# Kernel tuning notes

Hardware: AMD Instinct MI355X
Metric: run time of the kernel (lower is better)

## Reference

```python
import jax, jax.numpy as jnp
import numpy as np

EMBED_DIM = 1024
N_HEADS = 16
HEAD_DIM = EMBED_DIM // N_HEADS
B, S = 2, 2048


def setup_inputs() -> dict:
    key = jax.random.key(0)
    ks = jax.random.split(key, 8)
    scale = 1.0 / np.sqrt(EMBED_DIM)
    return {
        "key": jax.random.normal(ks[0], (B, S, EMBED_DIM), jnp.float32),
        "query": jax.random.normal(ks[1], (B, S, EMBED_DIM), jnp.float32),
        "value": jax.random.normal(ks[2], (B, S, EMBED_DIM), jnp.float32),
        # nn.Linear weights stored [out_features, in_features], applied as x @ W.T
        "Wq": jax.random.normal(ks[3], (EMBED_DIM, EMBED_DIM), jnp.float32) * scale,
        "Wk": jax.random.normal(ks[4], (EMBED_DIM, EMBED_DIM), jnp.float32) * scale,
        "Wv": jax.random.normal(ks[5], (EMBED_DIM, EMBED_DIM), jnp.float32) * scale,
        "Wo": jax.random.normal(ks[6], (EMBED_DIM, EMBED_DIM), jnp.float32) * scale,
        "bo": jax.random.normal(ks[7], (EMBED_DIM,), jnp.float32) * scale,
    }


def reference(key, query, value, Wq, Wk, Wv, Wo, bo) -> jnp.ndarray:
    b = key.shape[0]
    # project and split heads: [B, S, E] -> [B, H, S, D]
    def split_heads(x):
        return x.reshape(b, -1, N_HEADS, HEAD_DIM).transpose(0, 2, 1, 3)
    q = split_heads(query @ Wq.T)
    k = split_heads(key @ Wk.T)
    v = split_heads(value @ Wv.T)
    scores = jnp.einsum("bhqd,bhkd->bhqk", q, k) / np.sqrt(HEAD_DIM)
    attn = jax.nn.softmax(scores, axis=-1)
    ctx = jnp.einsum("bhqk,bhkd->bhqd", attn, v)  # [B, H, S, D]
    ctx = ctx.transpose(0, 2, 1, 3).reshape(b, -1, EMBED_DIM)
    return ctx @ Wo.T + bo
```

## Files before the change

### kernel.cpp

```cpp
#include <hip/hip_runtime.h>

typedef unsigned short u16;
typedef __bf16 bf8 __attribute__((ext_vector_type(8)));
typedef __bf16 bf2 __attribute__((ext_vector_type(2)));
typedef float f4 __attribute__((ext_vector_type(4)));

typedef __attribute__((address_space(1))) const unsigned int gas_u32;
typedef __attribute__((address_space(3))) unsigned int las_u32;
#define ASYNC16(g, l) __builtin_amdgcn_global_load_lds((gas_u32*)(g), (las_u32*)(l), 16, 0, 0)

__device__ __forceinline__ unsigned pkbf(float lo, float hi) {
    union { bf2 v; unsigned u; } t;
    t.v[0] = (__bf16)lo;
    t.v[1] = (__bf16)hi;
    return t.u;
}

__device__ __forceinline__ u16 bf1(float f) {
    union { __bf16 v; u16 u; } t;
    t.v = (__bf16)f;
    return t.u;
}

__device__ __forceinline__ float fexp2(float x) {
#if __has_builtin(__builtin_amdgcn_exp2f)
  return __builtin_amdgcn_exp2f(x);
#else
  return __expf(x * 0.69314718056f);
#endif
}

__global__ __launch_bounds__(256) void cvt_all(
    const float* __restrict__ k_, const float* __restrict__ q_, const float* __restrict__ v_,
    const float* __restrict__ wq, const float* __restrict__ wk, const float* __restrict__ wv,
    const float* __restrict__ wo, u16* __restrict__ ws) {
  size_t e = ((size_t)blockIdx.x * 256 + threadIdx.x) * 8;
  const float* src;
  if      (e <  4194304) src = k_ + e;
  else if (e <  8388608) src = q_ + (e - 4194304);
  else if (e < 12582912) src = v_ + (e - 8388608);
  else if (e < 13631488) src = wq + (e - 12582912);
  else if (e < 14680064) src = wk + (e - 13631488);
  else if (e < 15728640) src = wv + (e - 14680064);
  else                   src = wo + (e - 15728640);
  float4 f0 = ((const float4*)src)[0];
  float4 f1 = ((const float4*)src)[1];
  uint4 o;
  o.x = pkbf(f0.x, f0.y);
  o.y = pkbf(f0.z, f0.w);
  o.z = pkbf(f1.x, f1.y);
  o.w = pkbf(f1.z, f1.w);
  *(uint4*)(ws + e) = o;
}

template<int BM, bool FINAL>
__device__ __forceinline__ void gemm_tile(const u16* __restrict__ A, const u16* __restrict__ Bm,
                                          u16* __restrict__ Cb, float* __restrict__ Cf,
                                          const float* __restrict__ bias, float scale,
                                          int bm, int bn, int ldc) {
  __shared__ u16 As[BM*64];
  __shared__ u16 Bs[128*64];
  const int tid = threadIdx.x;
  const int wave = tid >> 6, lane = tid & 63;
  const int wm = wave >> 1, wn = wave & 1;
  const int quad = lane >> 4, l16 = lane & 15;
  const int MI = BM / 32;

  f4 acc[MI][4];
  const f4 zz = {0.f, 0.f, 0.f, 0.f};
  #pragma unroll
  for (int i = 0; i < MI; i++)
    #pragma unroll
    for (int j = 0; j < 4; j++) acc[i][j] = zz;

  const int kr = tid >> 3;
  const int cs = (tid & 7) ^ (kr & 7);
  const u16* ga = A  + (size_t)(bm*BM  + kr)*1024 + cs*8;
  const u16* gb = Bm + (size_t)(bn*128 + kr)*1024 + cs*8;
  u16* la = As + tid*8;
  u16* lb = Bs + tid*8;

  for (int kt = 0; kt < 1024; kt += 64) {
    #pragma unroll
    for (int p = 0; p < BM/32; p++) ASYNC16(ga + (size_t)(p*32)*1024 + kt, la + p*2048);
    #pragma unroll
    for (int p = 0; p < 4; p++)     ASYNC16(gb + (size_t)(p*32)*1024 + kt, lb + p*2048);
    __syncthreads();
    #pragma unroll
    for (int kk = 0; kk < 2; kk++) {
      bf8 af[MI];
      #pragma unroll
      for (int mi = 0; mi < MI; mi++)
        af[mi] = *(const bf8*)(As + (wm*(BM/2) + mi*16 + l16)*64 + (((kk*4 + quad) ^ (l16 & 7))*8));
      #pragma unroll
      for (int ni = 0; ni < 4; ni++) {
        bf8 bfr = *(const bf8*)(Bs + (wn*64 + ni*16 + l16)*64 + (((kk*4 + quad) ^ (l16 & 7))*8));
        #pragma unroll
        for (int mi = 0; mi < MI; mi++)
          acc[mi][ni] = __builtin_amdgcn_mfma_f32_16x16x32_bf16(af[mi], bfr, acc[mi][ni], 0, 0, 0);
      }
    }
    __syncthreads();
  }

  #pragma unroll
  for (int mi = 0; mi < MI; mi++)
    #pragma unroll
    for (int ni = 0; ni < 4; ni++) {
      const int col = bn*128 + wn*64 + ni*16 + l16;
      #pragma unroll
      for (int r = 0; r < 4; r++) {
        const int row = bm*BM + wm*(BM/2) + mi*16 + quad*4 + r;
        if (FINAL) Cf[(size_t)row*ldc + col] = acc[mi][ni][r] + bias[col];
        else       Cb[(size_t)row*ldc + col] = bf1(acc[mi][ni][r] * scale);
      }
    }
}

#define QSCALE 0.180336880f

__global__ __launch_bounds__(256, 3) void gemm_qkv(
    const u16* __restrict__ xq, const u16* __restrict__ xk, const u16* __restrict__ xv,
    const u16* __restrict__ wq, const u16* __restrict__ wk, const u16* __restrict__ wv,
    u16* __restrict__ Qo, u16* __restrict__ Ko, u16* __restrict__ Vto) {
  if (blockIdx.z == 0)
    gemm_tile<128,false>(xq, wq, Qo, nullptr, nullptr, QSCALE, blockIdx.x, blockIdx.y, 1024);
  else if (blockIdx.z == 1)
    gemm_tile<128,false>(xk, wk, Ko, nullptr, nullptr, 1.0f, blockIdx.x, blockIdx.y, 1024);
  else
    gemm_tile<128,false>(wv, xv, Vto, nullptr, nullptr, 1.0f, blockIdx.y, blockIdx.x, 4096);
}

__global__ __launch_bounds__(256, 2) void gemm_out(
    const u16* __restrict__ ctx, const u16* __restrict__ wo,
    const float* __restrict__ bias, float* __restrict__ out) {
  gemm_tile<64,true>(ctx, wo, nullptr, out, bias, 1.0f, blockIdx.x, blockIdx.y, 1024);
}

__global__ __launch_bounds__(256, 4) void flash_attn(
    const u16* __restrict__ Qg, const u16* __restrict__ Kg,
    const u16* __restrict__ Vtg, u16* __restrict__ ctx) {
  __shared__ uint4 smem4[2208];
  u16* Ks = (u16*)smem4;
  u16* Vt = (u16*)smem4 + 8192;
  float* Of = (float*)smem4;
  float* Lf = (float*)smem4 + 2*64*68;

  const int tid = threadIdx.x;
  const int wave = tid >> 6, lane = tid & 63;
  const int quad = lane >> 4, l16 = lane & 15;
  const int wq = wave >> 1, wk = wave & 1;
  const int h = blockIdx.x, qt = blockIdx.y, b = blockIdx.z;

  bf8 qf[2][2];
  {
    const u16* qp = Qg + (size_t)(b*2048 + qt*64 + wq*32)*1024 + h*64;
    #pragma unroll
    for (int qs = 0; qs < 2; qs++)
      #pragma unroll
      for (int kc = 0; kc < 2; kc++)
        qf[qs][kc] = *(const bf8*)(qp + (size_t)(qs*16 + l16)*1024 + kc*32 + quad*8);
  }

  const f4 zz = {0.f, 0.f, 0.f, 0.f};
  f4 ot[4][2];
  float lrow[2] = {0.f, 0.f};
  #pragma unroll
  for (int ds = 0; ds < 4; ds++)
    #pragma unroll
    for (int qs = 0; qs < 2; qs++) ot[ds][qs] = zz;

  const int kr = tid >> 3;
  const u16* kga = Kg + (size_t)(b*2048 + kr)*1024 + h*64 + ((tid & 7) ^ (kr & 7))*8;
  const int vd = tid >> 4;
  const u16* vga = Vtg + (size_t)(h*64 + vd)*4096 + b*2048 + (((tid & 15) ^ vd))*8;
  u16* kld = Ks + tid*8;
  u16* vld = Vt + tid*8;

  const int prow0 = ((l16 >> 2) << 3) + (l16 & 3);
  const int prow1 = prow0 + 4;

  for (int kv0 = 0; kv0 < 2048; kv0 += 128) {
    __syncthreads();
    #pragma unroll
    for (int p = 0; p < 4; p++) ASYNC16(kga + (size_t)(kv0 + p*32)*1024, kld + p*2048);
    #pragma unroll
    for (int p = 0; p < 4; p++) ASYNC16(vga + (size_t)(p*16)*4096 + kv0, vld + p*2048);
    __syncthreads();

    #pragma unroll
    for (int kb = 0; kb < 2; kb++) {
      f4 st[2][2];
      #pragma unroll
      for (int f = 0; f < 2; f++)
        #pragma unroll
        for (int qs = 0; qs < 2; qs++) st[f][qs] = zz;
      __builtin_amdgcn_s_setprio(1);
      #pragma unroll
      for (int f = 0; f < 2; f++) {
        const int row = wk*64 + kb*32 + (f ? prow1 : prow0);
        #pragma unroll
        for (int kc = 0; kc < 2; kc++) {
          bf8 kf = *(const bf8*)(Ks + row*64 + (((kc*4 + quad) ^ (row & 7))*8));
          #pragma unroll
          for (int qs = 0; qs < 2; qs++)
            st[f][qs] = __builtin_amdgcn_mfma_f32_16x16x32_bf16(kf, qf[qs][kc], st[f][qs], 0, 0, 0);
        }
      }
      __builtin_amdgcn_s_setprio(0);
      bf8 pf[2];
      #pragma unroll
      for (int qs = 0; qs < 2; qs++) {
        float p0 = fexp2(st[0][qs][0]), p1 = fexp2(st[0][qs][1]);
        float p2 = fexp2(st[0][qs][2]), p3 = fexp2(st[0][qs][3]);
        float p4 = fexp2(st[1][qs][0]), p5 = fexp2(st[1][qs][1]);
        float p6 = fexp2(st[1][qs][2]), p7 = fexp2(st[1][qs][3]);
        lrow[qs] += ((p0 + p1) + (p2 + p3)) + ((p4 + p5) + (p6 + p7));
        union { uint4 u; bf8 v; } pu;
        pu.u.x = pkbf(p0, p1);
        pu.u.y = pkbf(p2, p3);
        pu.u.z = pkbf(p4, p5);
        pu.u.w = pkbf(p6, p7);
        pf[qs] = pu.v;
      }
      __builtin_amdgcn_s_setprio(1);
      #pragma unroll
      for (int ds = 0; ds < 4; ds++) {
        const int d = ds*16 + l16;
        bf8 vf = *(const bf8*)(Vt + d*128 + (((wk*8 + kb*4 + quad) ^ l16)*8));
        #pragma unroll
        for (int qs = 0; qs < 2; qs++)
          ot[ds][qs] = __builtin_amdgcn_mfma_f32_16x16x32_bf16(vf, pf[qs], ot[ds][qs], 0, 0, 0);
      }
      __builtin_amdgcn_s_setprio(0);
    }
  }

  __syncthreads();
  #pragma unroll
  for (int qs = 0; qs < 2; qs++) {
    lrow[qs] += __shfl_xor(lrow[qs], 16);
    lrow[qs] += __shfl_xor(lrow[qs], 32);
  }
  float* Ofw = Of + wk*(64*68);
  #pragma unroll
  for (int ds = 0; ds < 4; ds++)
    #pragma unroll
    for (int qs = 0; qs < 2; qs++)
      #pragma unroll
      for (int r = 0; r < 4; r++)
        Ofw[(wq*32 + qs*16 + l16)*68 + ds*16 + quad*4 + r] = ot[ds][qs][r];
  if (quad == 0) {
    Lf[wk*64 + wq*32 + l16]      = lrow[0];
    Lf[wk*64 + wq*32 + 16 + l16] = lrow[1];
  }
  __syncthreads();
  {
    const int qr = tid >> 2, dp = (tid & 3)*16;
    const float inv = 1.f / (Lf[qr] + Lf[64 + qr]);
    const float* o0 = Of + qr*68 + dp;
    const float* o1 = o0 + 64*68;
    unsigned ow[8];
    #pragma unroll
    for (int i = 0; i < 8; i++)
      ow[i] = pkbf((o0[2*i] + o1[2*i]) * inv, (o0[2*i+1] + o1[2*i+1]) * inv);
    u16* cp = ctx + (size_t)(b*2048 + qt*64 + qr)*1024 + h*64 + dp;
    *(uint4*)cp       = *(uint4*)&ow[0];
    *(uint4*)(cp + 8) = *(uint4*)&ow[4];
  }
}

extern "C" void kernel_launch(void* const* d_in, const int* in_sizes, int n_in,
                              void* d_out, int out_size, void* d_ws, size_t ws_size,
                              hipStream_t stream) {
  const float* key_  = (const float*)d_in[0];
  const float* query = (const float*)d_in[1];
  const float* value = (const float*)d_in[2];
  const float* Wq = (const float*)d_in[3];
  const float* Wk = (const float*)d_in[4];
  const float* Wv = (const float*)d_in[5];
  const float* Wo = (const float*)d_in[6];
  const float* bo = (const float*)d_in[7];
  float* out = (float*)d_out;

  u16* ws  = (u16*)d_ws;
  u16* xkb = ws;
  u16* xqb = ws + 4194304;
  u16* xvb = ws + 8388608;
  u16* Wqb = ws + 12582912;
  u16* Wkb = ws + 13631488;
  u16* Wvb = ws + 14680064;
  u16* Wob = ws + 15728640;
  u16* Qb  = ws + 16777216;
  u16* Kb  = ws + 20971520;
  u16* Vtb = ws + 25165824;
  u16* Cb  = ws + 29360128;

  cvt_all<<<8192, 256, 0, stream>>>(key_, query, value, Wq, Wk, Wv, Wo, ws);
  gemm_qkv<<<dim3(32, 8, 3), 256, 0, stream>>>(xqb, xkb, xvb, Wqb, Wkb, Wvb, Qb, Kb, Vtb);
  flash_attn<<<dim3(16, 32, 2), 256, 0, stream>>>(Qb, Kb, Vtb, Cb);
  gemm_out<<<dim3(64, 8), 256, 0, stream>>>(Cb, Wob, bo, out);
}
```

Measured before the change: 203.1 us.

## Load K and V fragments directly from global memory into registers in flash attention

Removes the LDS staging of K and V tiles, along with the block-wide barriers around each tile load. Each wave now reads its own K and V MFMA fragments straight from global memory into registers, in a loop unrolled by two to overlap loads with compute. The aim is to cut LDS traffic and synchronisation. In exchange, the four waves of a block no longer share K/V tiles, so global and L2 reads rise and latency hiding now depends on the compiler's scheduling.

```diff
diff --git a/kernel.cpp b/kernel.cpp
--- a/kernel.cpp
+++ b/kernel.cpp
@@ -140,11 +140,9 @@
 __global__ __launch_bounds__(256, 4) void flash_attn(
     const u16* __restrict__ Qg, const u16* __restrict__ Kg,
     const u16* __restrict__ Vtg, u16* __restrict__ ctx) {
-  __shared__ uint4 smem4[2208];
-  u16* Ks = (u16*)smem4;
-  u16* Vt = (u16*)smem4 + 8192;
-  float* Of = (float*)smem4;
-  float* Lf = (float*)smem4 + 2*64*68;
+  __shared__ float Os[2*64*68 + 128];
+  float* Of = Os;
+  float* Lf = Os + 2*64*68;
 
   const int tid = threadIdx.x;
   const int wave = tid >> 6, lane = tid & 63;
@@ -170,73 +168,63 @@
     #pragma unroll
     for (int qs = 0; qs < 2; qs++) ot[ds][qs] = zz;
 
-  const int kr = tid >> 3;
-  const u16* kga = Kg + (size_t)(b*2048 + kr)*1024 + h*64 + ((tid & 7) ^ (kr & 7))*8;
-  const int vd = tid >> 4;
-  const u16* vga = Vtg + (size_t)(h*64 + vd)*4096 + b*2048 + (((tid & 15) ^ vd))*8;
-  u16* kld = Ks + tid*8;
-  u16* vld = Vt + tid*8;
-
   const int prow0 = ((l16 >> 2) << 3) + (l16 & 3);
-  const int prow1 = prow0 + 4;
-
-  for (int kv0 = 0; kv0 < 2048; kv0 += 128) {
-    __syncthreads();
-    #pragma unroll
-    for (int p = 0; p < 4; p++) ASYNC16(kga + (size_t)(kv0 + p*32)*1024, kld + p*2048);
-    #pragma unroll
-    for (int p = 0; p < 4; p++) ASYNC16(vga + (size_t)(p*16)*4096 + kv0, vld + p*2048);
-    __syncthreads();
-
-    #pragma unroll
-    for (int kb = 0; kb < 2; kb++) {
-      f4 st[2][2];
-      #pragma unroll
-      for (int f = 0; f < 2; f++)
-        #pragma unroll
-        for (int qs = 0; qs < 2; qs++) st[f][qs] = zz;
-      __builtin_amdgcn_s_setprio(1);
-      #pragma unroll
-      for (int f = 0; f < 2; f++) {
-        const int row = wk*64 + kb*32 + (f ? prow1 : prow0);
-        #pragma unroll
-        for (int kc = 0; kc < 2; kc++) {
-          bf8 kf = *(const bf8*)(Ks + row*64 + (((kc*4 + quad) ^ (row & 7))*8));
-          #pragma unroll
-          for (int qs = 0; qs < 2; qs++)
-            st[f][qs] = __builtin_amdgcn_mfma_f32_16x16x32_bf16(kf, qf[qs][kc], st[f][qs], 0, 0, 0);
-        }
-      }
-      __builtin_amdgcn_s_setprio(0);
-      bf8 pf[2];
-      #pragma unroll
-      for (int qs = 0; qs < 2; qs++) {
-        float p0 = fexp2(st[0][qs][0]), p1 = fexp2(st[0][qs][1]);
-        float p2 = fexp2(st[0][qs][2]), p3 = fexp2(st[0][qs][3]);
-        float p4 = fexp2(st[1][qs][0]), p5 = fexp2(st[1][qs][1]);
-        float p6 = fexp2(st[1][qs][2]), p7 = fexp2(st[1][qs][3]);
-        lrow[qs] += ((p0 + p1) + (p2 + p3)) + ((p4 + p5) + (p6 + p7));
-        union { uint4 u; bf8 v; } pu;
-        pu.u.x = pkbf(p0, p1);
-        pu.u.y = pkbf(p2, p3);
-        pu.u.z = pkbf(p4, p5);
-        pu.u.w = pkbf(p6, p7);
-        pf[qs] = pu.v;
-      }
-      __builtin_amdgcn_s_setprio(1);
-      #pragma unroll
-      for (int ds = 0; ds < 4; ds++) {
-        const int d = ds*16 + l16;
-        bf8 vf = *(const bf8*)(Vt + d*128 + (((wk*8 + kb*4 + quad) ^ l16)*8));
+
+  const u16* kp = Kg + (size_t)(b*2048 + wk*32 + prow0)*1024 + h*64 + quad*8;
+  const u16* vp = Vtg + (size_t)(h*64 + l16)*4096 + b*2048 + wk*32 + quad*8;
+
+  #pragma unroll 2
+  for (int t = 0; t < 32; t++) {
+    const u16* kpt = kp + (size_t)t*65536;
+    const u16* vpt = vp + t*64;
+    bf8 kf[2][2], vfr[4];
+    #pragma unroll
+    for (int f = 0; f < 2; f++)
+      #pragma unroll
+      for (int kc = 0; kc < 2; kc++)
+        kf[f][kc] = *(const bf8*)(kpt + f*4096 + kc*32);
+    #pragma unroll
+    for (int ds = 0; ds < 4; ds++)
+      vfr[ds] = *(const bf8*)(vpt + (size_t)(ds*16)*4096);
+
+    f4 st[2][2];
+    #pragma unroll
+    for (int f = 0; f < 2; f++)
+      #pragma unroll
+      for (int qs = 0; qs < 2; qs++) st[f][qs] = zz;
+    __builtin_amdgcn_s_setprio(1);
+    #pragma unroll
+    for (int f = 0; f < 2; f++)
+      #pragma unroll
+      for (int kc = 0; kc < 2; kc++)
         #pragma unroll
         for (int qs = 0; qs < 2; qs++)
-          ot[ds][qs] = __builtin_amdgcn_mfma_f32_16x16x32_bf16(vf, pf[qs], ot[ds][qs], 0, 0, 0);
-      }
-      __builtin_amdgcn_s_setprio(0);
+          st[f][qs] = __builtin_amdgcn_mfma_f32_16x16x32_bf16(kf[f][kc], qf[qs][kc], st[f][qs], 0, 0, 0);
+    __builtin_amdgcn_s_setprio(0);
+    bf8 pf[2];
+    #pragma unroll
+    for (int qs = 0; qs < 2; qs++) {
+      float p0 = fexp2(st[0][qs][0]), p1 = fexp2(st[0][qs][1]);
+      float p2 = fexp2(st[0][qs][2]), p3 = fexp2(st[0][qs][3]);
+      float p4 = fexp2(st[1][qs][0]), p5 = fexp2(st[1][qs][1]);
+      float p6 = fexp2(st[1][qs][2]), p7 = fexp2(st[1][qs][3]);
+      lrow[qs] += ((p0 + p1) + (p2 + p3)) + ((p4 + p5) + (p6 + p7));
+      union { uint4 u; bf8 v; } pu;
+      pu.u.x = pkbf(p0, p1);
+      pu.u.y = pkbf(p2, p3);
+      pu.u.z = pkbf(p4, p5);
+      pu.u.w = pkbf(p6, p7);
+      pf[qs] = pu.v;
     }
-  }
-
-  __syncthreads();
+    __builtin_amdgcn_s_setprio(1);
+    #pragma unroll
+    for (int ds = 0; ds < 4; ds++)
+      #pragma unroll
+      for (int qs = 0; qs < 2; qs++)
+        ot[ds][qs] = __builtin_amdgcn_mfma_f32_16x16x32_bf16(vfr[ds], pf[qs], ot[ds][qs], 0, 0, 0);
+    __builtin_amdgcn_s_setprio(0);
+  }
+
   #pragma unroll
   for (int qs = 0; qs < 2; qs++) {
     lrow[qs] += __shfl_xor(lrow[qs], 16);
```

Measured after the change: 281.9 us. 38.8% more time.
